# Kernel tuning notes

Measured on AMD Instinct MI355X. Metric: run time of the kernel, lower is better.

## Reference

```python
import jax, jax.numpy as jnp
import numpy as np

N = 500000      # examples = M * (nr+1)
K = 20          # context set size (indices[:, 3:])
NR = 24         # negatives per positive
H = 128         # hidden_channels == node feature dim
NODES = 10000   # ingredient vocabulary


def setup_inputs() -> dict:
    key = jax.random.key(0)
    ks = jax.random.split(key, 6)
    indices = jax.random.randint(ks[0], (N, 3 + K), 0, NODES)
    x = jax.random.normal(ks[1], (NODES, H), dtype=jnp.float32)
    scale = 0.02
    W1 = jax.random.normal(ks[2], (H, 3 * H), dtype=jnp.float32) * scale
    b1 = jnp.zeros((H,), jnp.float32)
    W2 = jax.random.normal(ks[3], (H // 2, H), dtype=jnp.float32) * scale
    b2 = jnp.zeros((H // 2,), jnp.float32)
    W3 = jax.random.normal(ks[4], (1, H // 2), dtype=jnp.float32) * scale
    b3 = jnp.zeros((1,), jnp.float32)
    return {"indices": indices, "nr": NR, "x": x,
            "W1": W1, "b1": b1, "W2": W2, "b2": b2, "W3": W3, "b3": b3}


def _embed_context(ctx_idx, x, nr):
    # ctx_idx: [N, K]; one context row per group of (nr+1) examples
    new_idx = ctx_idx[:-1:nr + 1]                 # [M, K]
    emb = x[new_idx]                               # [M, K, H] gather
    s = emb.sum(axis=1)                            # [M, H]
    norm = jnp.maximum((new_idx > 0).sum(axis=1), 1).astype(x.dtype)[:, None]
    mean = s / norm                                # masked mean over context
    return jnp.repeat(mean, nr + 1, axis=0)        # broadcast back to [N, H]


def reference(indices, nr, x, W1, b1, W2, b2, W3, b3):
    ing1 = x[indices[:, 0]]                        # [N, H]
    ing2 = x[indices[:, 1]]                        # [N, H]
    set_emb = _embed_context(indices[:, 3:], x, nr)  # [N, H]
    y = jnp.concatenate([ing1, ing2, set_emb], axis=1)  # [N, 3H]
    y = jax.nn.relu(y @ W1.T + b1)
    y = jax.nn.relu(y @ W2.T + b2)
    return y @ W3.T + b3                           # [N, 1]
```

## Files before the change

kernel.cpp:

```cpp
#include <hip/hip_runtime.h>
#include <hip/hip_bf16.h>

#define N_ROWS   500000
#define NR1      25
#define NGROUPS  20000
#define KCTX     20
#define H        128
#define NODES    10000
#define IDX_COLS 23

#define NT       4
#define RPB      (NT * 128)
#define MAXG     22

typedef __attribute__((ext_vector_type(8))) short short8;
typedef __attribute__((ext_vector_type(4))) float f32x4;

__device__ __forceinline__ unsigned pkbf(float lo, float hi) {
  __hip_bfloat162 h = __float22bfloat162_rn(make_float2(lo, hi));
  union { __hip_bfloat162 h; unsigned u; } c; c.h = h;
  return c.u;
}
__device__ __forceinline__ float bf2f(unsigned short u) {
  union { unsigned u; float f; } c; c.u = ((unsigned)u) << 16; return c.f;
}

#define PN 64
#define PRE_BLOCKS ((NODES + PN - 1) / PN)
__global__ __launch_bounds__(256) void k_precompute(
    const float* __restrict__ x, const float* __restrict__ W1,
    const int* __restrict__ indices,
    unsigned short* __restrict__ Pb, int2* __restrict__ idx2) {
  const int tid = threadIdx.x;
  const int m   = blockIdx.y;

  if (m == 3) {
    const int stride = PRE_BLOCKS * 256;
    for (int r = blockIdx.x * 256 + tid; r < N_ROWS; r += stride) {
      idx2[r] = make_int2(indices[(size_t)r * IDX_COLS + 0],
                          indices[(size_t)r * IDX_COLS + 1]);
    }
    return;
  }

  __shared__ short wlds[128][136];
  const int tbase = blockIdx.x * PN;

#pragma unroll
  for (int it = 0; it < 16; ++it) {
    const int f  = it * 256 + tid;
    const int j  = f >> 5;
    const int q4 = f & 31;
    const float4 v = *(const float4*)(W1 + (size_t)j * (3 * H) + m * H + q4 * 4);
    *(unsigned*)&wlds[j][q4 * 4]     = pkbf(v.x, v.y);
    *(unsigned*)&wlds[j][q4 * 4 + 2] = pkbf(v.z, v.w);
  }
  __syncthreads();

  const int lane = tid & 63;
  const int wv   = tid >> 6;
  const int col  = lane & 15;
  const int quad = lane >> 4;

  int node = tbase + wv * 16 + col;
  if (node > NODES - 1) node = NODES - 1;
  const float4* __restrict__ xr = (const float4*)(x + (size_t)node * H);

  short8 Af[4];
#pragma unroll
  for (int kt = 0; kt < 4; ++kt) {
    const int f4 = kt * 8 + quad * 2;
    const float4 v0 = xr[f4], v1 = xr[f4 + 1];
    union { short8 v; unsigned u[4]; } pk;
    pk.u[0] = pkbf(v0.x, v0.y);
    pk.u[1] = pkbf(v0.z, v0.w);
    pk.u[2] = pkbf(v1.x, v1.y);
    pk.u[3] = pkbf(v1.z, v1.w);
    Af[kt] = pk.v;
  }

  f32x4 acc[8];
#pragma unroll
  for (int ct = 0; ct < 8; ++ct) acc[ct] = (f32x4)(0.f);

#pragma unroll
  for (int kt = 0; kt < 4; ++kt) {
#pragma unroll
    for (int ct = 0; ct < 8; ++ct) {
      const short8 Bf = *(const short8*)&wlds[ct * 16 + col][kt * 32 + quad * 8];
      acc[ct] = __builtin_amdgcn_mfma_f32_16x16x32_bf16(Af[kt], Bf, acc[ct], 0, 0, 0);
    }
  }

  unsigned short* __restrict__ Pm = Pb + (size_t)m * NODES * H;
#pragma unroll
  for (int reg = 0; reg < 4; ++reg) {
    const int n = tbase + wv * 16 + quad * 4 + reg;
    if (n < NODES) {
#pragma unroll
      for (int ct = 0; ct < 8; ++ct) {
        union { unsigned u; unsigned short s[2]; } c;
        c.u = pkbf(acc[ct][reg], 0.f);
        Pm[(size_t)n * H + ct * 16 + col] = c.s[0];
      }
    }
  }
}

__global__ __launch_bounds__(256) void k_main(
    const int* __restrict__ indices, const int2* __restrict__ idx2,
    const unsigned short* __restrict__ P1b, const unsigned short* __restrict__ P2b,
    const unsigned short* __restrict__ P3b,
    const float* __restrict__ W2, const float* __restrict__ b1,
    const float* __restrict__ b2, const float* __restrict__ W3,
    const float* __restrict__ b3, float* __restrict__ out) {
  __shared__ short w2s[64][136];
  __shared__ float cgs[MAXG][132];

  const int tid   = threadIdx.x;
  const int rbase = blockIdx.x * RPB;
  const int gbase = rbase / NR1;

  for (int idx = tid; idx < 64 * 64; idx += 256) {
    const int n  = idx >> 6;
    const int kp = idx & 63;
    const float2 w = *(const float2*)(W2 + (size_t)n * H + kp * 2);
    *(unsigned*)&w2s[n][kp * 2] = pkbf(w.x, w.y);
  }

  {
    int rlast = rbase + RPB - 1; if (rlast > N_ROWS - 1) rlast = N_ROWS - 1;
    const int G   = rlast / NR1 - gbase + 1;
    const int jj  = (tid & 63) * 2;
    const int sub = tid >> 6;
    const float2 b1v = *(const float2*)(b1 + jj);
#pragma unroll
    for (int it = 0; it < 6; ++it) {
      const int gi = it * 4 + sub;
      if (gi < G) {
        const int* __restrict__ rowidx =
            indices + (size_t)(gbase + gi) * NR1 * IDX_COLS + 3;
        float s0 = 0.f, s1 = 0.f;
        int cnt = 0;
#pragma unroll
        for (int c = 0; c < KCTX; ++c) {
          const int idx = rowidx[c];
          const unsigned w = *(const unsigned*)(P3b + (size_t)idx * H + jj);
          s0 += bf2f((unsigned short)(w & 0xffffu));
          s1 += bf2f((unsigned short)(w >> 16));
          cnt += (idx > 0) ? 1 : 0;
        }
        const float rn = 1.f / (float)((cnt > 1) ? cnt : 1);
        cgs[gi][jj]     = b1v.x + s0 * rn;
        cgs[gi][jj + 1] = b1v.y + s1 * rn;
      }
    }
  }
  __syncthreads();

  const int lane = tid & 63;
  const int wv   = tid >> 6;
  const int col  = lane & 15;
  const int quad = lane >> 4;

  float b2v[4], w3v[4];
#pragma unroll
  for (int ct = 0; ct < 4; ++ct) {
    b2v[ct] = b2[ct * 16 + col];
    w3v[ct] = W3[ct * 16 + col];
  }
  const float bias3 = b3[0];

  short8 ua[2][2][4], ub[2][2][4];
  int    gl[2][2];

  {
    const int R = rbase + wv * 32;
#pragma unroll
    for (int rt = 0; rt < 2; ++rt) {
      const int r  = R + rt * 16 + col;
      const int rc = (r < N_ROWS) ? r : (N_ROWS - 1);
      const int2 ii = idx2[rc];
      const short8* __restrict__ pa = (const short8*)(P1b + (size_t)ii.x * H);
      const short8* __restrict__ pb = (const short8*)(P2b + (size_t)ii.y * H);
#pragma unroll
      for (int kt = 0; kt < 4; ++kt) {
        ua[0][rt][kt] = pa[kt * 4 + quad];
        ub[0][rt][kt] = pb[kt * 4 + quad];
      }
      gl[0][rt] = rc / NR1 - gbase;
    }
  }

#pragma unroll
  for (int t = 0; t < NT; ++t) {
    const int cur = t & 1;
    const int nxt = cur ^ 1;
    const int Rt  = rbase + t * 128 + wv * 32;

    short8 A[2][4];
#pragma unroll
    for (int rt = 0; rt < 2; ++rt) {
#pragma unroll
      for (int kt = 0; kt < 4; ++kt) {
        union { short8 v; unsigned short s[8]; } va, vb;
        va.v = ua[cur][rt][kt];
        vb.v = ub[cur][rt][kt];
        const float4 c0 = *(const float4*)&cgs[gl[cur][rt]][kt * 32 + quad * 8];
        const float4 c1 = *(const float4*)&cgs[gl[cur][rt]][kt * 32 + quad * 8 + 4];
        const float h0 = fmaxf(bf2f(va.s[0]) + bf2f(vb.s[0]) + c0.x, 0.f);
        const float h1 = fmaxf(bf2f(va.s[1]) + bf2f(vb.s[1]) + c0.y, 0.f);
        const float h2 = fmaxf(bf2f(va.s[2]) + bf2f(vb.s[2]) + c0.z, 0.f);
        const float h3 = fmaxf(bf2f(va.s[3]) + bf2f(vb.s[3]) + c0.w, 0.f);
        const float h4 = fmaxf(bf2f(va.s[4]) + bf2f(vb.s[4]) + c1.x, 0.f);
        const float h5 = fmaxf(bf2f(va.s[5]) + bf2f(vb.s[5]) + c1.y, 0.f);
        const float h6 = fmaxf(bf2f(va.s[6]) + bf2f(vb.s[6]) + c1.z, 0.f);
        const float h7 = fmaxf(bf2f(va.s[7]) + bf2f(vb.s[7]) + c1.w, 0.f);
        union { short8 v; unsigned u[4]; } pk;
        pk.u[0] = pkbf(h0, h1);
        pk.u[1] = pkbf(h2, h3);
        pk.u[2] = pkbf(h4, h5);
        pk.u[3] = pkbf(h6, h7);
        A[rt][kt] = pk.v;
      }
    }

    if (t + 1 < NT) {
      const int Rn = rbase + (t + 1) * 128 + wv * 32;
#pragma unroll
      for (int rt = 0; rt < 2; ++rt) {
        const int r  = Rn + rt * 16 + col;
        const int rc = (r < N_ROWS) ? r : (N_ROWS - 1);
        const int2 ii = idx2[rc];
        const short8* __restrict__ pa = (const short8*)(P1b + (size_t)ii.x * H);
        const short8* __restrict__ pb = (const short8*)(P2b + (size_t)ii.y * H);
#pragma unroll
        for (int kt = 0; kt < 4; ++kt) {
          ua[nxt][rt][kt] = pa[kt * 4 + quad];
          ub[nxt][rt][kt] = pb[kt * 4 + quad];
        }
        gl[nxt][rt] = rc / NR1 - gbase;
      }
    }

    f32x4 acc[2][4];
#pragma unroll
    for (int rt = 0; rt < 2; ++rt)
#pragma unroll
      for (int ct = 0; ct < 4; ++ct) acc[rt][ct] = (f32x4)(0.f);
#pragma unroll
    for (int kt = 0; kt < 4; ++kt) {
#pragma unroll
      for (int ct = 0; ct < 4; ++ct) {
        const short8 Bf = *(const short8*)&w2s[ct * 16 + col][kt * 32 + quad * 8];
#pragma unroll
        for (int rt = 0; rt < 2; ++rt)
          acc[rt][ct] = __builtin_amdgcn_mfma_f32_16x16x32_bf16(
              A[rt][kt], Bf, acc[rt][ct], 0, 0, 0);
      }
    }
#pragma unroll
    for (int rt = 0; rt < 2; ++rt) {
#pragma unroll
      for (int reg = 0; reg < 4; ++reg) {
        float s = 0.f;
#pragma unroll
        for (int ct = 0; ct < 4; ++ct)
          s += fmaxf(acc[rt][ct][reg] + b2v[ct], 0.f) * w3v[ct];
        s += __shfl_xor(s, 1);
        s += __shfl_xor(s, 2);
        s += __shfl_xor(s, 4);
        s += __shfl_xor(s, 8);
        if (col == 0) {
          const int row = Rt + rt * 16 + quad * 4 + reg;
          if (row < N_ROWS) out[row] = s + bias3;
        }
      }
    }
  }
}

extern "C" void kernel_launch(void* const* d_in, const int* in_sizes, int n_in,
                              void* d_out, int out_size, void* d_ws, size_t ws_size,
                              hipStream_t stream) {
  const int*   indices = (const int*)  d_in[0];
  const float* x  = (const float*)d_in[2];
  const float* W1 = (const float*)d_in[3];
  const float* b1 = (const float*)d_in[4];
  const float* W2 = (const float*)d_in[5];
  const float* b2 = (const float*)d_in[6];
  const float* W3 = (const float*)d_in[7];
  const float* b3 = (const float*)d_in[8];
  float* out = (float*)d_out;

  unsigned short* Pb  = (unsigned short*)d_ws;
  unsigned short* P1b = Pb;
  unsigned short* P2b = Pb + (size_t)NODES * H;
  unsigned short* P3b = Pb + (size_t)2 * NODES * H;
  int2* idx2 = (int2*)(Pb + (size_t)3 * NODES * H);

  dim3 gpre(PRE_BLOCKS, 4);
  k_precompute<<<gpre, 256, 0, stream>>>(x, W1, indices, Pb, idx2);
  k_main<<<(N_ROWS + RPB - 1) / RPB, 256, 0, stream>>>(indices, idx2,
                                                       P1b, P2b, P3b,
                                                       W2, b1, b2, W3, b3, out);
}
```

Before: 158.0 us.

## Precompute per-group context projection once in precompute kernel, gather it in main

The per-group context embedding is now computed once per group in the precompute kernel. It averages the fp32 context rows and multiplies by the W1 slice with MFMA, adding b1, instead of every main block re-summing projected bf16 rows into shared memory. The main kernel drops its shared-memory context stage and gathers a third bf16 row per example from the new group table. Rows per block are halved and idx2 packing is spread across the spare precompute blocks. The third gather per row adds global traffic to the main loop. The slice P3 is still computed but no longer used.

```diff
diff --git a/kernel.cpp b/kernel.cpp
--- a/kernel.cpp
+++ b/kernel.cpp
@@ -9,9 +9,7 @@
 #define NODES    10000
 #define IDX_COLS 23
 
-#define NT       4
-#define RPB      (NT * 128)
-#define MAXG     22
+#define RPB      256
 
 typedef __attribute__((ext_vector_type(8))) short short8;
 typedef __attribute__((ext_vector_type(4))) float f32x4;
@@ -26,17 +24,22 @@
 }
 
 #define PN 64
-#define PRE_BLOCKS ((NODES + PN - 1) / PN)
+#define PRE_BLOCKS  ((NODES + PN - 1) / PN)
+#define GPB 64
+#define CTX_BLOCKS  ((NGROUPS + GPB - 1) / GPB)
+#define PACK_BLOCKS (3 * (CTX_BLOCKS - PRE_BLOCKS))
 __global__ __launch_bounds__(256) void k_precompute(
     const float* __restrict__ x, const float* __restrict__ W1,
-    const int* __restrict__ indices,
-    unsigned short* __restrict__ Pb, int2* __restrict__ idx2) {
+    const int* __restrict__ indices, const float* __restrict__ b1,
+    unsigned short* __restrict__ Pb, unsigned short* __restrict__ Cgb,
+    int2* __restrict__ idx2) {
   const int tid = threadIdx.x;
   const int m   = blockIdx.y;
 
-  if (m == 3) {
-    const int stride = PRE_BLOCKS * 256;
-    for (int r = blockIdx.x * 256 + tid; r < N_ROWS; r += stride) {
+  if (m < 3 && blockIdx.x >= PRE_BLOCKS) {
+    const int pid = m * (CTX_BLOCKS - PRE_BLOCKS) + (blockIdx.x - PRE_BLOCKS);
+    const int stride = PACK_BLOCKS * 256;
+    for (int r = pid * 256 + tid; r < N_ROWS; r += stride) {
       idx2[r] = make_int2(indices[(size_t)r * IDX_COLS + 0],
                           indices[(size_t)r * IDX_COLS + 1]);
     }
@@ -44,14 +47,14 @@
   }
 
   __shared__ short wlds[128][136];
-  const int tbase = blockIdx.x * PN;
-
+
+  const int ms = (m == 3) ? 2 : m;
 #pragma unroll
   for (int it = 0; it < 16; ++it) {
     const int f  = it * 256 + tid;
     const int j  = f >> 5;
     const int q4 = f & 31;
-    const float4 v = *(const float4*)(W1 + (size_t)j * (3 * H) + m * H + q4 * 4);
+    const float4 v = *(const float4*)(W1 + (size_t)j * (3 * H) + ms * H + q4 * 4);
     *(unsigned*)&wlds[j][q4 * 4]     = pkbf(v.x, v.y);
     *(unsigned*)&wlds[j][q4 * 4 + 2] = pkbf(v.z, v.w);
   }
@@ -62,21 +65,54 @@
   const int col  = lane & 15;
   const int quad = lane >> 4;
 
-  int node = tbase + wv * 16 + col;
-  if (node > NODES - 1) node = NODES - 1;
-  const float4* __restrict__ xr = (const float4*)(x + (size_t)node * H);
-
   short8 Af[4];
-#pragma unroll
-  for (int kt = 0; kt < 4; ++kt) {
-    const int f4 = kt * 8 + quad * 2;
-    const float4 v0 = xr[f4], v1 = xr[f4 + 1];
-    union { short8 v; unsigned u[4]; } pk;
-    pk.u[0] = pkbf(v0.x, v0.y);
-    pk.u[1] = pkbf(v0.z, v0.w);
-    pk.u[2] = pkbf(v1.x, v1.y);
-    pk.u[3] = pkbf(v1.z, v1.w);
-    Af[kt] = pk.v;
+  if (m < 3) {
+    int node = blockIdx.x * PN + wv * 16 + col;
+    if (node > NODES - 1) node = NODES - 1;
+    const float4* __restrict__ xr = (const float4*)(x + (size_t)node * H);
+#pragma unroll
+    for (int kt = 0; kt < 4; ++kt) {
+      const int f4 = kt * 8 + quad * 2;
+      const float4 v0 = xr[f4], v1 = xr[f4 + 1];
+      union { short8 v; unsigned u[4]; } pk;
+      pk.u[0] = pkbf(v0.x, v0.y);
+      pk.u[1] = pkbf(v0.z, v0.w);
+      pk.u[2] = pkbf(v1.x, v1.y);
+      pk.u[3] = pkbf(v1.z, v1.w);
+      Af[kt] = pk.v;
+    }
+  } else {
+    int g = blockIdx.x * GPB + wv * 16 + col;
+    if (g > NGROUPS - 1) g = NGROUPS - 1;
+    const int* __restrict__ rowidx = indices + (size_t)g * NR1 * IDX_COLS + 3;
+    int idxs[KCTX];
+    int cnt = 0;
+#pragma unroll
+    for (int c = 0; c < KCTX; ++c) {
+      idxs[c] = rowidx[c];
+      cnt += (idxs[c] > 0) ? 1 : 0;
+    }
+    const float rn = 1.f / (float)((cnt > 1) ? cnt : 1);
+#pragma unroll
+    for (int kt = 0; kt < 4; ++kt) {
+      float s[8];
+#pragma unroll
+      for (int e = 0; e < 8; ++e) s[e] = 0.f;
+#pragma unroll
+      for (int c = 0; c < KCTX; ++c) {
+        const float4* __restrict__ xr =
+            (const float4*)(x + (size_t)idxs[c] * H + kt * 32 + quad * 8);
+        const float4 v0 = xr[0], v1 = xr[1];
+        s[0] += v0.x; s[1] += v0.y; s[2] += v0.z; s[3] += v0.w;
+        s[4] += v1.x; s[5] += v1.y; s[6] += v1.z; s[7] += v1.w;
+      }
+      union { short8 v; unsigned u[4]; } pk;
+      pk.u[0] = pkbf(s[0] * rn, s[1] * rn);
+      pk.u[1] = pkbf(s[2] * rn, s[3] * rn);
+      pk.u[2] = pkbf(s[4] * rn, s[5] * rn);
+      pk.u[3] = pkbf(s[6] * rn, s[7] * rn);
+      Af[kt] = pk.v;
+    }
   }
 
   f32x4 acc[8];
@@ -92,34 +128,50 @@
     }
   }
 
-  unsigned short* __restrict__ Pm = Pb + (size_t)m * NODES * H;
-#pragma unroll
-  for (int reg = 0; reg < 4; ++reg) {
-    const int n = tbase + wv * 16 + quad * 4 + reg;
-    if (n < NODES) {
-#pragma unroll
-      for (int ct = 0; ct < 8; ++ct) {
-        union { unsigned u; unsigned short s[2]; } c;
-        c.u = pkbf(acc[ct][reg], 0.f);
-        Pm[(size_t)n * H + ct * 16 + col] = c.s[0];
+  if (m < 3) {
+    unsigned short* __restrict__ Pm = Pb + (size_t)m * NODES * H;
+#pragma unroll
+    for (int reg = 0; reg < 4; ++reg) {
+      const int n = blockIdx.x * PN + wv * 16 + quad * 4 + reg;
+      if (n < NODES) {
+#pragma unroll
+        for (int ct = 0; ct < 8; ++ct) {
+          union { unsigned u; unsigned short s[2]; } c;
+          c.u = pkbf(acc[ct][reg], 0.f);
+          Pm[(size_t)n * H + ct * 16 + col] = c.s[0];
+        }
+      }
+    }
+  } else {
+    float b1v[8];
+#pragma unroll
+    for (int ct = 0; ct < 8; ++ct) b1v[ct] = b1[ct * 16 + col];
+#pragma unroll
+    for (int reg = 0; reg < 4; ++reg) {
+      const int g = blockIdx.x * GPB + wv * 16 + quad * 4 + reg;
+      if (g < NGROUPS) {
+#pragma unroll
+        for (int ct = 0; ct < 8; ++ct) {
+          union { unsigned u; unsigned short s[2]; } c;
+          c.u = pkbf(acc[ct][reg] + b1v[ct], 0.f);
+          Cgb[(size_t)g * H + ct * 16 + col] = c.s[0];
+        }
       }
     }
   }
 }
 
 __global__ __launch_bounds__(256) void k_main(
-    const int* __restrict__ indices, const int2* __restrict__ idx2,
+    const int2* __restrict__ idx2,
     const unsigned short* __restrict__ P1b, const unsigned short* __restrict__ P2b,
-    const unsigned short* __restrict__ P3b,
-    const float* __restrict__ W2, const float* __restrict__ b1,
-    const float* __restrict__ b2, const float* __restrict__ W3,
-    const float* __restrict__ b3, float* __restrict__ out) {
+    const unsigned short* __restrict__ Cgb,
+    const float* __restrict__ W2, const float* __restrict__ b2,
+    const float* __restrict__ W3, const float* __restrict__ b3,
+    float* __restrict__ out) {
   __shared__ short w2s[64][136];
-  __shared__ float cgs[MAXG][132];
 
   const int tid   = threadIdx.x;
   const int rbase = blockIdx.x * RPB;
-  const int gbase = rbase / NR1;
 
   for (int idx = tid; idx < 64 * 64; idx += 256) {
     const int n  = idx >> 6;
@@ -127,35 +179,6 @@
     const float2 w = *(const float2*)(W2 + (size_t)n * H + kp * 2);
     *(unsigned*)&w2s[n][kp * 2] = pkbf(w.x, w.y);
   }
-
-  {
-    int rlast = rbase + RPB - 1; if (rlast > N_ROWS - 1) rlast = N_ROWS - 1;
-    const int G   = rlast / NR1 - gbase + 1;
-    const int jj  = (tid & 63) * 2;
-    const int sub = tid >> 6;
-    const float2 b1v = *(const float2*)(b1 + jj);
-#pragma unroll
-    for (int it = 0; it < 6; ++it) {
-      const int gi = it * 4 + sub;
-      if (gi < G) {
-        const int* __restrict__ rowidx =
-            indices + (size_t)(gbase + gi) * NR1 * IDX_COLS + 3;
-        float s0 = 0.f, s1 = 0.f;
-        int cnt = 0;
-#pragma unroll
-        for (int c = 0; c < KCTX; ++c) {
-          const int idx = rowidx[c];
-          const unsigned w = *(const unsigned*)(P3b + (size_t)idx * H + jj);
-          s0 += bf2f((unsigned short)(w & 0xffffu));
-          s1 += bf2f((unsigned short)(w >> 16));
-          cnt += (idx > 0) ? 1 : 0;
-        }
-        const float rn = 1.f / (float)((cnt > 1) ? cnt : 1);
-        cgs[gi][jj]     = b1v.x + s0 * rn;
-        cgs[gi][jj + 1] = b1v.y + s1 * rn;
-      }
-    }
-  }
   __syncthreads();
 
   const int lane = tid & 63;
@@ -171,8 +194,7 @@
   }
   const float bias3 = b3[0];
 
-  short8 ua[2][2][4], ub[2][2][4];
-  int    gl[2][2];
+  short8 ua[2][2][4], ub[2][2][4], uc[2][2][4];
 
   {
     const int R = rbase + wv * 32;
@@ -181,19 +203,21 @@
       const int r  = R + rt * 16 + col;
       const int rc = (r < N_ROWS) ? r : (N_ROWS - 1);
       const int2 ii = idx2[rc];
+      const int g   = rc / NR1;
       const short8* __restrict__ pa = (const short8*)(P1b + (size_t)ii.x * H);
       const short8* __restrict__ pb = (const short8*)(P2b + (size_t)ii.y * H);
+      const short8* __restrict__ pc = (const short8*)(Cgb + (size_t)g * H);
 #pragma unroll
       for (int kt = 0; kt < 4; ++kt) {
         ua[0][rt][kt] = pa[kt * 4 + quad];
         ub[0][rt][kt] = pb[kt * 4 + quad];
-      }
-      gl[0][rt] = rc / NR1 - gbase;
-    }
-  }
-
-#pragma unroll
-  for (int t = 0; t < NT; ++t) {
+        uc[0][rt][kt] = pc[kt * 4 + quad];
+      }
+    }
+  }
+
+#pragma unroll
+  for (int t = 0; t < 2; ++t) {
     const int cur = t & 1;
     const int nxt = cur ^ 1;
     const int Rt  = rbase + t * 128 + wv * 32;
@@ -203,43 +227,40 @@
     for (int rt = 0; rt < 2; ++rt) {
 #pragma unroll
       for (int kt = 0; kt < 4; ++kt) {
-        union { short8 v; unsigned short s[8]; } va, vb;
+        union { short8 v; unsigned short s[8]; } va, vb, vc;
         va.v = ua[cur][rt][kt];
         vb.v = ub[cur][rt][kt];
-        const float4 c0 = *(const float4*)&cgs[gl[cur][rt]][kt * 32 + quad * 8];
-        const float4 c1 = *(const float4*)&cgs[gl[cur][rt]][kt * 32 + quad * 8 + 4];
-        const float h0 = fmaxf(bf2f(va.s[0]) + bf2f(vb.s[0]) + c0.x, 0.f);
-        const float h1 = fmaxf(bf2f(va.s[1]) + bf2f(vb.s[1]) + c0.y, 0.f);
-        const float h2 = fmaxf(bf2f(va.s[2]) + bf2f(vb.s[2]) + c0.z, 0.f);
-        const float h3 = fmaxf(bf2f(va.s[3]) + bf2f(vb.s[3]) + c0.w, 0.f);
-        const float h4 = fmaxf(bf2f(va.s[4]) + bf2f(vb.s[4]) + c1.x, 0.f);
-        const float h5 = fmaxf(bf2f(va.s[5]) + bf2f(vb.s[5]) + c1.y, 0.f);
-        const float h6 = fmaxf(bf2f(va.s[6]) + bf2f(vb.s[6]) + c1.z, 0.f);
-        const float h7 = fmaxf(bf2f(va.s[7]) + bf2f(vb.s[7]) + c1.w, 0.f);
+        vc.v = uc[cur][rt][kt];
         union { short8 v; unsigned u[4]; } pk;
-        pk.u[0] = pkbf(h0, h1);
-        pk.u[1] = pkbf(h2, h3);
-        pk.u[2] = pkbf(h4, h5);
-        pk.u[3] = pkbf(h6, h7);
+#pragma unroll
+        for (int e = 0; e < 4; ++e) {
+          const float h0 = fmaxf(bf2f(va.s[2 * e])     + bf2f(vb.s[2 * e])
+                                 + bf2f(vc.s[2 * e]), 0.f);
+          const float h1 = fmaxf(bf2f(va.s[2 * e + 1]) + bf2f(vb.s[2 * e + 1])
+                                 + bf2f(vc.s[2 * e + 1]), 0.f);
+          pk.u[e] = pkbf(h0, h1);
+        }
         A[rt][kt] = pk.v;
       }
     }
 
-    if (t + 1 < NT) {
+    if (t + 1 < 2) {
       const int Rn = rbase + (t + 1) * 128 + wv * 32;
 #pragma unroll
       for (int rt = 0; rt < 2; ++rt) {
         const int r  = Rn + rt * 16 + col;
         const int rc = (r < N_ROWS) ? r : (N_ROWS - 1);
         const int2 ii = idx2[rc];
+        const int g   = rc / NR1;
         const short8* __restrict__ pa = (const short8*)(P1b + (size_t)ii.x * H);
         const short8* __restrict__ pb = (const short8*)(P2b + (size_t)ii.y * H);
+        const short8* __restrict__ pc = (const short8*)(Cgb + (size_t)g * H);
 #pragma unroll
         for (int kt = 0; kt < 4; ++kt) {
           ua[nxt][rt][kt] = pa[kt * 4 + quad];
           ub[nxt][rt][kt] = pb[kt * 4 + quad];
-        }
-        gl[nxt][rt] = rc / NR1 - gbase;
+          uc[nxt][rt][kt] = pc[kt * 4 + quad];
+        }
       }
     }
 
@@ -296,12 +317,11 @@
   unsigned short* Pb  = (unsigned short*)d_ws;
   unsigned short* P1b = Pb;
   unsigned short* P2b = Pb + (size_t)NODES * H;
-  unsigned short* P3b = Pb + (size_t)2 * NODES * H;
-  int2* idx2 = (int2*)(Pb + (size_t)3 * NODES * H);
-
-  dim3 gpre(PRE_BLOCKS, 4);
-  k_precompute<<<gpre, 256, 0, stream>>>(x, W1, indices, Pb, idx2);
-  k_main<<<(N_ROWS + RPB - 1) / RPB, 256, 0, stream>>>(indices, idx2,
-                                                       P1b, P2b, P3b,
-                                                       W2, b1, b2, W3, b3, out);
-}
+  unsigned short* Cgb = Pb + (size_t)3 * NODES * H;
+  int2* idx2 = (int2*)(Cgb + (size_t)NGROUPS * H);
+
+  dim3 gpre(CTX_BLOCKS, 4);
+  k_precompute<<<gpre, 256, 0, stream>>>(x, W1, indices, b1, Pb, Cgb, idx2);
+  k_main<<<(N_ROWS + RPB - 1) / RPB, 256, 0, stream>>>(idx2, P1b, P2b, Cgb,
+                                                       W2, b2, W3, b3, out);
+}
```

Result: slower. 191.9 us (+21.4%).
